# Performance work log

Measured on AMD Instinct MI355X. Metric: run time of the kernel, lower is better.

Reference implementation:

```python
import jax, jax.numpy as jnp
import numpy as np

V, NSEG, MAXLEN, D, H = 32000, 2, 512, 768, 12
HS = D // H  # head_size = 64
B, T, NMASK = 16, 512, 20
LN_EPS = 1e-5


def setup_inputs() -> dict:
    key = jax.random.key(0)
    ks = jax.random.split(key, 16)
    s = 0.02
    return {
        "sequence": jax.random.randint(ks[0], (B, T), 0, V),
        "segment": jax.random.randint(ks[1], (B, T), 0, NSEG),
        "attn_mask": jax.random.randint(ks[2], (B, T), 0, 2).astype(jnp.int32),
        "masked_pos": jax.random.randint(ks[3], (B, NMASK), 0, T),
        "tok_emb": jax.random.normal(ks[4], (V, D), jnp.float32) * s,
        "seg_emb": jax.random.normal(ks[5], (NSEG, D), jnp.float32) * s,
        "pos_emb": jax.random.normal(ks[6], (MAXLEN, D), jnp.float32) * s,
        "ln_g": jnp.ones((D,), jnp.float32),
        "ln_b": jnp.zeros((D,), jnp.float32),
        "Wq": jax.random.normal(ks[7], (H, D, HS), jnp.float32) * s,
        "Wk": jax.random.normal(ks[8], (H, D, HS), jnp.float32) * s,
        "Wv": jax.random.normal(ks[9], (H, D, HS), jnp.float32) * s,
        "W_lm": jax.random.normal(ks[10], (D, V), jnp.float32) * s,
        "b_lm": jnp.zeros((V,), jnp.float32),
        "W_cls": jax.random.normal(ks[11], (D, 2), jnp.float32) * s,
        "b_cls": jnp.zeros((2,), jnp.float32),
    }


def reference(sequence, segment, attn_mask, masked_pos,
              tok_emb, seg_emb, pos_emb, ln_g, ln_b,
              Wq, Wk, Wv, W_lm, b_lm, W_cls, b_cls):
    Tlen = sequence.shape[1]
    # --- BERTEmbedding (dropout = identity in eval) ---
    emb = tok_emb[sequence] + seg_emb[segment] + pos_emb[jnp.arange(Tlen)][None]  # [B,T,D]
    mu = jnp.mean(emb, axis=-1, keepdims=True)
    var = jnp.mean(jnp.square(emb - mu), axis=-1, keepdims=True)
    x = (emb - mu) * jax.lax.rsqrt(var + LN_EPS) * ln_g + ln_b  # [B,T,D]

    # --- Multi-head attention (heads batched instead of Python loop) ---
    q = jnp.einsum('btd,hds->bhts', x, Wq)
    k = jnp.einsum('btd,hds->bhts', x, Wk)
    v = jnp.einsum('btd,hds->bhts', x, Wv)
    wei = jnp.einsum('bhts,bhus->bhtu', q, k) * (HS ** -0.5)  # [B,H,T,T]
    # original: wei.masked_fill(attn_mask[:, :, None] == 0, -1e-11) -> masks over query dim
    wei = jnp.where(attn_mask[:, None, :, None] == 0, jnp.float32(-1e-11), wei)
    wei = jax.nn.softmax(wei, axis=-1)
    out = jnp.einsum('bhtu,bhus->bhts', wei, v)  # [B,H,T,HS]
    x = out.transpose(0, 2, 1, 3).reshape(out.shape[0], Tlen, H * HS)  # cat heads -> [B,T,D]

    # --- Output heads ---
    x_masked = jnp.take_along_axis(x, masked_pos[:, :, None], axis=1)  # [B,NMASK,D]
    logits_lm = x_masked @ W_lm + b_lm          # [B,NMASK,V]
    logits_clsf = x[:, 0, :] @ W_cls + b_cls    # [B,2]
    return (logits_lm, logits_clsf)
```

## Files before the change

kernel.cpp:

```cpp
#include <hip/hip_runtime.h>
#include <hip/hip_bf16.h>

#define V_     32000
#define NSEG_  2
#define MAXLEN_ 512
#define D_     768
#define H_     12
#define HS_    64
#define B_     16
#define T_     512
#define NMASK_ 20
#define LN_EPS_ 1e-5f

typedef __hip_bfloat16 bf16;
typedef unsigned short ushortT;
typedef __attribute__((ext_vector_type(8))) short short8;
typedef __attribute__((ext_vector_type(4))) float f32x4;
typedef __attribute__((ext_vector_type(4))) unsigned int u32x4;
typedef __attribute__((ext_vector_type(4))) unsigned short u16x4;

__device__ __forceinline__ ushortT f2bu(float f) {
    bf16 h = __float2bfloat16(f);
    return *reinterpret_cast<ushortT*>(&h);
}

__global__ void k_embed_ln(const int* __restrict__ seq, const int* __restrict__ seg,
                           const float* __restrict__ tok, const float* __restrict__ sege,
                           const float* __restrict__ pos, const float* __restrict__ g,
                           const float* __restrict__ bb, ushortT* __restrict__ xb) {
    int row = blockIdx.x;
    int t = row & (T_ - 1);
    int tid = threadIdx.x;
    __shared__ float wsum[3], wsq[3];

    int sidx = seq[row];
    int gidx = seg[row];

    f32x4 e = *(const f32x4*)(tok  + (size_t)sidx * D_ + tid * 4);
    f32x4 e2 = *(const f32x4*)(sege + (size_t)gidx * D_ + tid * 4);
    f32x4 e3 = *(const f32x4*)(pos  + (size_t)t    * D_ + tid * 4);
    e = e + e2 + e3;

    float ls = e.x + e.y + e.z + e.w;
    float lq = e.x * e.x + e.y * e.y + e.z * e.z + e.w * e.w;
    #pragma unroll
    for (int o = 32; o > 0; o >>= 1) {
        ls += __shfl_down(ls, o);
        lq += __shfl_down(lq, o);
    }
    if ((tid & 63) == 0) { wsum[tid >> 6] = ls; wsq[tid >> 6] = lq; }
    __syncthreads();
    float s  = wsum[0] + wsum[1] + wsum[2];
    float sq = wsq[0] + wsq[1] + wsq[2];
    float mean = s * (1.0f / D_);
    float var  = sq * (1.0f / D_) - mean * mean;
    float rstd = rsqrtf(var + LN_EPS_);

    f32x4 g4 = *(const f32x4*)(g  + tid * 4);
    f32x4 b4 = *(const f32x4*)(bb + tid * 4);
    f32x4 x4;
    x4.x = (e.x - mean) * rstd * g4.x + b4.x;
    x4.y = (e.y - mean) * rstd * g4.y + b4.y;
    x4.z = (e.z - mean) * rstd * g4.z + b4.z;
    x4.w = (e.w - mean) * rstd * g4.w + b4.w;
    u16x4 ov = {f2bu(x4.x), f2bu(x4.y), f2bu(x4.z), f2bu(x4.w)};
    *(u16x4*)(xb + (size_t)row * D_ + tid * 4) = ov;
}

__global__ void k_prep_wqkv(const float* __restrict__ Wq, const float* __restrict__ Wk,
                            const float* __restrict__ Wv, ushortT* __restrict__ Wt) {
    int blk = blockIdx.x;
    int which = blk / H_, h = blk % H_;
    int kc = blockIdx.y * 64;
    const float* W = (which == 0) ? Wq : (which == 1) ? Wk : Wv;
    __shared__ float tile[64][65];
    int tid = threadIdx.x, c = tid & 63, rgrp = tid >> 6;
    for (int kk = rgrp; kk < 64; kk += 4)
        tile[kk][c] = W[((size_t)h * D_ + kc + kk) * HS_ + c];
    __syncthreads();
    for (int ss = rgrp; ss < 64; ss += 4)
        Wt[((size_t)which * D_ + h * HS_ + ss) * D_ + kc + c] = f2bu(tile[c][ss]);
}

__global__ void k_transpose_lm(const float* __restrict__ W, ushortT* __restrict__ Wt) {
    __shared__ float tile[64][65];
    int v0 = blockIdx.x * 64, d0 = blockIdx.y * 64;
    int tid = threadIdx.x, c = tid & 63;
    for (int rr = tid >> 6; rr < 64; rr += 4)
        tile[rr][c] = W[(size_t)(d0 + rr) * V_ + v0 + c];
    __syncthreads();
    for (int rr = tid >> 6; rr < 64; rr += 4)
        Wt[(size_t)(v0 + rr) * D_ + d0 + c] = f2bu(tile[c][rr]);
}

__global__ void k_gather_xm(const float* __restrict__ x2, const int* __restrict__ masked_pos,
                            ushortT* __restrict__ xm) {
    int r = blockIdx.x;
    int tid = threadIdx.x;
    if (r < B_ * NMASK_) {
        int b = r / NMASK_, m = r % NMASK_;
        int t = masked_pos[b * NMASK_ + m];
        for (int d = tid; d < D_; d += 256)
            xm[(size_t)r * D_ + d] = f2bu(x2[((size_t)b * T_ + t) * D_ + d]);
    } else {
        for (int d = tid; d < D_; d += 256)
            xm[(size_t)r * D_ + d] = 0;
    }
}

__device__ __forceinline__ void stage_tile(const ushortT* __restrict__ A,
                                           const ushortT* __restrict__ Bt,
                                           int m0, int n0, int k0,
                                           ushortT* As, ushortT* Bs,
                                           int w, int lane) {
    #pragma unroll
    for (int i = 0; i < 2; ++i) {
        int slot = w * 64 + lane + i * 256;
        int row = slot >> 2;
        int cs = ((slot & 3) ^ (row & 3)) * 8;
        __builtin_amdgcn_global_load_lds(
            (const __attribute__((address_space(1))) void*)(A + (size_t)(m0 + row) * D_ + k0 + cs),
            (__attribute__((address_space(3))) void*)(As + (w * 64 + i * 256) * 8),
            16, 0, 0);
        __builtin_amdgcn_global_load_lds(
            (const __attribute__((address_space(1))) void*)(Bt + (size_t)(n0 + row) * D_ + k0 + cs),
            (__attribute__((address_space(3))) void*)(Bs + (w * 64 + i * 256) * 8),
            16, 0, 0);
    }
}

__device__ __forceinline__ void gemm128_2ph(const ushortT* __restrict__ A,
                                            const ushortT* __restrict__ Bt,
                                            int m0, int n0,
                                            ushortT* lds,
                                            f32x4 acc[4][4]) {
    const int NT = D_ / 32;
    int tid = threadIdx.x;
    int lane = tid & 63, w = tid >> 6;
    int wr = (w >> 1) * 64, wc = (w & 1) * 64;
    int l16 = lane & 15, lk = lane >> 4;
    int sw = (lk ^ (l16 & 3)) * 8;

    #pragma unroll
    for (int i = 0; i < 4; ++i)
        #pragma unroll
        for (int j = 0; j < 4; ++j)
            acc[i][j] = (f32x4){0.f, 0.f, 0.f, 0.f};

    stage_tile(A, Bt, m0, n0, 0, lds, lds + 4096, w, lane);
    asm volatile("s_waitcnt vmcnt(0)" ::: "memory");
    __builtin_amdgcn_s_barrier();

    for (int t = 0; t < NT; ++t) {
        int cur = (t & 1) * 8192;
        int nxt = 8192 - cur;
        if (t + 1 < NT)
            stage_tile(A, Bt, m0, n0, (t + 1) * 32, lds + nxt, lds + nxt + 4096, w, lane);

        const ushortT* Asc = lds + cur;
        const ushortT* Bsc = lds + cur + 4096;
        short8 a[4], bfr[4];
        #pragma unroll
        for (int i = 0; i < 4; ++i) {
            a[i]   = *(const short8*)(Asc + (wr + i * 16 + l16) * 32 + sw);
            bfr[i] = *(const short8*)(Bsc + (wc + i * 16 + l16) * 32 + sw);
        }
        #pragma unroll
        for (int i = 0; i < 4; ++i)
            #pragma unroll
            for (int j = 0; j < 4; ++j)
                acc[i][j] = __builtin_amdgcn_mfma_f32_16x16x32_bf16(a[i], bfr[j], acc[i][j], 0, 0, 0);

        asm volatile("s_waitcnt vmcnt(0)" ::: "memory");
        __builtin_amdgcn_s_barrier();
    }
}

__global__ __launch_bounds__(256, 4)
void k_gemm_qkv(const ushortT* __restrict__ xb, const ushortT* __restrict__ WcatT,
                ushortT* __restrict__ qb, ushortT* __restrict__ kb,
                ushortT* __restrict__ vb) {
    __shared__ ushortT lds[128 * 136];
    f32x4 acc[4][4];
    int lin = (blockIdx.x & 7) * 144 + (blockIdx.x >> 3);
    int n0 = (lin % 18) * 128, m0 = (lin / 18) * 128;
    gemm128_2ph(xb, WcatT, m0, n0, lds, acc);

    int tid = threadIdx.x;
    int lane = tid & 63, w = tid >> 6;
    int wr = (w >> 1) * 64, wc = (w & 1) * 64;
    int l16 = lane & 15, lk = lane >> 4;

    #pragma unroll
    for (int j = 0; j < 4; ++j) {
        int n = wc + j * 16 + l16;
        #pragma unroll
        for (int i = 0; i < 4; ++i) {
            #pragma unroll
            for (int r = 0; r < 4; ++r) {
                int m = wr + i * 16 + lk * 4 + r;
                lds[m * 136 + n] = f2bu(acc[i][j][r]);
            }
        }
    }
    __syncthreads();

    int which = n0 / D_;
    int nrem0 = n0 - which * D_;
    ushortT* outp = (which == 0) ? qb : (which == 1) ? kb : vb;
    int b = m0 >> 9;
    int t0 = m0 & (T_ - 1);
    #pragma unroll
    for (int p = 0; p < 8; ++p) {
        int chunk = p * 256 + tid;
        int row = chunk >> 4;
        int nc = (chunk & 15) * 8;
        int h = (nrem0 >> 6) + (nc >> 6);
        int s0 = nc & 63;
        u32x4 v = *(const u32x4*)(&lds[row * 136 + nc]);
        *(u32x4*)(outp + ((size_t)(b * H_ + h) * T_ + (t0 + row)) * HS_ + s0) = v;
    }
}

__global__ __launch_bounds__(256, 4)
void k_gemm_lm(const ushortT* __restrict__ xm, const ushortT* __restrict__ WlmT,
               const float* __restrict__ blm, float* __restrict__ out) {
    __shared__ ushortT lds[16384];
    f32x4 acc[4][4];
    int m0 = blockIdx.x * 128, n0 = blockIdx.y * 128;
    gemm128_2ph(xm, WlmT, m0, n0, lds, acc);

    int lane = threadIdx.x & 63, w = threadIdx.x >> 6;
    int wr = (w >> 1) * 64, wc = (w & 1) * 64;
    int l16 = lane & 15, lk = lane >> 4;
    #pragma unroll
    for (int j = 0; j < 4; ++j) {
        int n = n0 + wc + j * 16 + l16;
        float bias = blm[n];
        #pragma unroll
        for (int i = 0; i < 4; ++i) {
            #pragma unroll
            for (int r = 0; r < 4; ++r) {
                int m = m0 + wr + i * 16 + lk * 4 + r;
                if (m < B_ * NMASK_)
                    out[(size_t)m * V_ + n] = acc[i][j][r] + bias;
            }
        }
    }
}

__global__ __launch_bounds__(256, 4)
void k_attn_mfma(const ushortT* __restrict__ qb, const ushortT* __restrict__ kb,
                 const ushortT* __restrict__ vb, const int* __restrict__ attn_mask,
                 float* __restrict__ x2) {
    int lin = (blockIdx.x & 7) * 192 + (blockIdx.x >> 3);
    int qt = lin & 7, bh = lin >> 3;
    int b = bh / H_, h = bh % H_;
    int tid = threadIdx.x, lane = tid & 63, w = tid >> 6;
    int l16 = lane & 15, lk = lane >> 4;

    __shared__ ushortT QP[64][72];
    __shared__ ushortT Ks[64][72];
    __shared__ ushortT Vts[64][72];
    __shared__ float mskS[64];

    const ushortT* Qg = qb + ((size_t)bh * T_ + qt * 64) * HS_;
    #pragma unroll
    for (int i = 0; i < 2; ++i) {
        int slot = tid + i * 256;
        int r = slot >> 3, c8 = (slot & 7) * 8;
        *(u32x4*)(&QP[r][c8]) = *(const u32x4*)(Qg + (size_t)r * HS_ + c8);
    }
    if (tid < 64)
        mskS[tid] = attn_mask[b * T_ + qt * 64 + tid] ? 0.125f : 0.0f;
    __syncthreads();

    short8 aq[2];
    #pragma unroll
    for (int ks = 0; ks < 2; ++ks)
        aq[ks] = *(const short8*)(&QP[w * 16 + l16][ks * 32 + lk * 8]);
    float mrow[4];
    #pragma unroll
    for (int r = 0; r < 4; ++r)
        mrow[r] = mskS[w * 16 + lk * 4 + r];

    float lsum[4];
    f32x4 accO[4];
    #pragma unroll
    for (int r = 0; r < 4; ++r) lsum[r] = 0.f;
    #pragma unroll
    for (int j = 0; j < 4; ++j)
        accO[j] = (f32x4){0.f, 0.f, 0.f, 0.f};

    for (int kt = 0; kt < 8; ++kt) {
        __syncthreads();
        {
            int r = tid >> 2, c = (tid & 3) * 16;
            const ushortT* Kg = kb + ((size_t)bh * T_ + kt * 64 + r) * HS_ + c;
            *(u32x4*)(&Ks[r][c])     = *(const u32x4*)(Kg);
            *(u32x4*)(&Ks[r][c + 8]) = *(const u32x4*)(Kg + 8);
        }
        {
            int r = lane;
            int c = w * 16;
            const ushortT* Vg = vb + ((size_t)bh * T_ + kt * 64 + r) * HS_ + c;
            short8 v0 = *(const short8*)(Vg);
            short8 v1 = *(const short8*)(Vg + 8);
            #pragma unroll
            for (int e = 0; e < 8; ++e) Vts[c + e][r]     = (ushortT)v0[e];
            #pragma unroll
            for (int e = 0; e < 8; ++e) Vts[c + 8 + e][r] = (ushortT)v1[e];
        }
        __syncthreads();

        f32x4 accS[4];
        #pragma unroll
        for (int j = 0; j < 4; ++j)
            accS[j] = (f32x4){0.f, 0.f, 0.f, 0.f};
        #pragma unroll
        for (int ks = 0; ks < 2; ++ks) {
            short8 bk[4];
            #pragma unroll
            for (int j = 0; j < 4; ++j)
                bk[j] = *(const short8*)(&Ks[j * 16 + l16][ks * 32 + lk * 8]);
            #pragma unroll
            for (int j = 0; j < 4; ++j)
                accS[j] = __builtin_amdgcn_mfma_f32_16x16x32_bf16(aq[ks], bk[j], accS[j], 0, 0, 0);
        }

        #pragma unroll
        for (int r = 0; r < 4; ++r) {
            int rowl = lk * 4 + r;
            float m = mrow[r];
            float p0 = __expf(accS[0][r] * m);
            float p1 = __expf(accS[1][r] * m);
            float p2 = __expf(accS[2][r] * m);
            float p3 = __expf(accS[3][r] * m);
            lsum[r] += (p0 + p1) + (p2 + p3);
            QP[w * 16 + rowl][0 * 16 + l16] = f2bu(p0);
            QP[w * 16 + rowl][1 * 16 + l16] = f2bu(p1);
            QP[w * 16 + rowl][2 * 16 + l16] = f2bu(p2);
            QP[w * 16 + rowl][3 * 16 + l16] = f2bu(p3);
        }

        #pragma unroll
        for (int ks2 = 0; ks2 < 2; ++ks2) {
            short8 ap = *(const short8*)(&QP[w * 16 + l16][ks2 * 32 + lk * 8]);
            short8 bv[4];
            #pragma unroll
            for (int j = 0; j < 4; ++j)
                bv[j] = *(const short8*)(&Vts[j * 16 + l16][ks2 * 32 + lk * 8]);
            #pragma unroll
            for (int j = 0; j < 4; ++j)
                accO[j] = __builtin_amdgcn_mfma_f32_16x16x32_bf16(ap, bv[j], accO[j], 0, 0, 0);
        }
    }

    #pragma unroll
    for (int r = 0; r < 4; ++r) {
        float s = lsum[r];
        #pragma unroll
        for (int off = 1; off < 16; off <<= 1)
            s += __shfl_xor(s, off);
        float inv = 1.0f / s;
        int t = qt * 64 + w * 16 + lk * 4 + r;
        float* outp = x2 + ((size_t)b * T_ + t) * D_ + h * HS_;
        #pragma unroll
        for (int j = 0; j < 4; ++j)
            outp[j * 16 + l16] = accO[j][r] * inv;
    }
}

__global__ void k_cls(const float* __restrict__ x2, const float* __restrict__ Wc,
                      const float* __restrict__ bc, float* __restrict__ out) {
    int b = blockIdx.x;
    int tid = threadIdx.x;
    __shared__ float red0[4], red1[4];
    float a0 = 0.f, a1 = 0.f;
    const float* xr = x2 + (size_t)b * T_ * D_;
    for (int d = tid; d < D_; d += 256) {
        float x = xr[d];
        a0 += x * Wc[d * 2];
        a1 += x * Wc[d * 2 + 1];
    }
    #pragma unroll
    for (int o = 32; o > 0; o >>= 1) {
        a0 += __shfl_down(a0, o);
        a1 += __shfl_down(a1, o);
    }
    if ((tid & 63) == 0) { red0[tid >> 6] = a0; red1[tid >> 6] = a1; }
    __syncthreads();
    if (tid == 0)
        out[b * 2]     = red0[0] + red0[1] + red0[2] + red0[3] + bc[0];
    if (tid == 1)
        out[b * 2 + 1] = red1[0] + red1[1] + red1[2] + red1[3] + bc[1];
}

extern "C" void kernel_launch(void* const* d_in, const int* in_sizes, int n_in,
                              void* d_out, int out_size, void* d_ws, size_t ws_size,
                              hipStream_t stream) {
    const int* seq        = (const int*)d_in[0];
    const int* seg        = (const int*)d_in[1];
    const int* attn_mask  = (const int*)d_in[2];
    const int* masked_pos = (const int*)d_in[3];
    const float* tok  = (const float*)d_in[4];
    const float* sege = (const float*)d_in[5];
    const float* pos  = (const float*)d_in[6];
    const float* ln_g = (const float*)d_in[7];
    const float* ln_b = (const float*)d_in[8];
    const float* Wq   = (const float*)d_in[9];
    const float* Wk   = (const float*)d_in[10];
    const float* Wv   = (const float*)d_in[11];
    const float* Wlm  = (const float*)d_in[12];
    const float* blm  = (const float*)d_in[13];
    const float* Wc   = (const float*)d_in[14];
    const float* bc   = (const float*)d_in[15];

    float* out_lm  = (float*)d_out;
    float* out_cls = out_lm + (size_t)B_ * NMASK_ * V_;

    const size_t XSZ = (size_t)B_ * T_ * D_;
    float* ws = (float*)d_ws;
    float*   x2   = ws;
    ushortT* base = (ushortT*)(ws + XSZ);
    ushortT* xb    = base;
    ushortT* qb    = base + XSZ;
    ushortT* kb    = base + 2 * XSZ;
    ushortT* vb    = base + 3 * XSZ;
    ushortT* WcatT = base + 4 * XSZ;
    ushortT* WlmT  = base;
    ushortT* xm    = base + (size_t)V_ * D_;

    k_embed_ln<<<B_ * T_, 192, 0, stream>>>(seq, seg, tok, sege, pos, ln_g, ln_b, xb);
    k_prep_wqkv<<<dim3(3 * H_, 12), 256, 0, stream>>>(Wq, Wk, Wv, WcatT);
    k_gemm_qkv<<<1152, 256, 0, stream>>>(xb, WcatT, qb, kb, vb);
    k_attn_mfma<<<192 * 8, 256, 0, stream>>>(qb, kb, vb, attn_mask, x2);
    k_transpose_lm<<<dim3(V_ / 64, D_ / 64), 256, 0, stream>>>(Wlm, WlmT);
    k_gather_xm<<<384, 256, 0, stream>>>(x2, masked_pos, xm);
    k_gemm_lm<<<dim3(3, 250), 256, 0, stream>>>(xm, WlmT, blm, out_lm);
    k_cls<<<B_, 256, 0, stream>>>(x2, Wc, bc, out_cls);
}
```

Baseline: 163.4 us.

## Fuse LM weight transpose and bf16 conversion into LM GEMM loader

Removes the separate kernel that transposed and converted the 768x32000 fp32 LM weight to bf16. The LM GEMM now reads the fp32 weights directly, converts them to bf16 in registers and writes them transposed into padded LDS, overlapping these loads with the MFMA work. This avoids a full write and re-read of a bf16 copy of the weight. The trade-off is that each of the 3 M-blocks reads the fp32 weight itself (three times the fp32 traffic through L2), and the loads are scalar and strided by V rather than vector loads into LDS.

```diff
diff --git a/kernel.cpp b/kernel.cpp
--- a/kernel.cpp
+++ b/kernel.cpp
@@ -82,17 +82,6 @@
         Wt[((size_t)which * D_ + h * HS_ + ss) * D_ + kc + c] = f2bu(tile[c][ss]);
 }
 
-__global__ void k_transpose_lm(const float* __restrict__ W, ushortT* __restrict__ Wt) {
-    __shared__ float tile[64][65];
-    int v0 = blockIdx.x * 64, d0 = blockIdx.y * 64;
-    int tid = threadIdx.x, c = tid & 63;
-    for (int rr = tid >> 6; rr < 64; rr += 4)
-        tile[rr][c] = W[(size_t)(d0 + rr) * V_ + v0 + c];
-    __syncthreads();
-    for (int rr = tid >> 6; rr < 64; rr += 4)
-        Wt[(size_t)(v0 + rr) * D_ + d0 + c] = f2bu(tile[c][rr]);
-}
-
 __global__ void k_gather_xm(const float* __restrict__ x2, const int* __restrict__ masked_pos,
                             ushortT* __restrict__ xm) {
     int r = blockIdx.x;
@@ -108,23 +97,16 @@
     }
 }
 
-__device__ __forceinline__ void stage_tile(const ushortT* __restrict__ A,
-                                           const ushortT* __restrict__ Bt,
-                                           int m0, int n0, int k0,
-                                           ushortT* As, ushortT* Bs,
-                                           int w, int lane) {
+__device__ __forceinline__ void stage_chunk(const ushortT* __restrict__ src, int row_stride,
+                                            int r0, int k0, ushortT* dst, int w, int lane) {
     #pragma unroll
     for (int i = 0; i < 2; ++i) {
         int slot = w * 64 + lane + i * 256;
         int row = slot >> 2;
         int cs = ((slot & 3) ^ (row & 3)) * 8;
         __builtin_amdgcn_global_load_lds(
-            (const __attribute__((address_space(1))) void*)(A + (size_t)(m0 + row) * D_ + k0 + cs),
-            (__attribute__((address_space(3))) void*)(As + (w * 64 + i * 256) * 8),
-            16, 0, 0);
-        __builtin_amdgcn_global_load_lds(
-            (const __attribute__((address_space(1))) void*)(Bt + (size_t)(n0 + row) * D_ + k0 + cs),
-            (__attribute__((address_space(3))) void*)(Bs + (w * 64 + i * 256) * 8),
+            (const __attribute__((address_space(1))) void*)(src + (size_t)(r0 + row) * row_stride + k0 + cs),
+            (__attribute__((address_space(3))) void*)(dst + (w * 64 + i * 256) * 8),
             16, 0, 0);
     }
 }
@@ -147,15 +129,18 @@
         for (int j = 0; j < 4; ++j)
             acc[i][j] = (f32x4){0.f, 0.f, 0.f, 0.f};
 
-    stage_tile(A, Bt, m0, n0, 0, lds, lds + 4096, w, lane);
+    stage_chunk(A, D_, m0, 0, lds, w, lane);
+    stage_chunk(Bt, D_, n0, 0, lds + 4096, w, lane);
     asm volatile("s_waitcnt vmcnt(0)" ::: "memory");
     __builtin_amdgcn_s_barrier();
 
     for (int t = 0; t < NT; ++t) {
         int cur = (t & 1) * 8192;
         int nxt = 8192 - cur;
-        if (t + 1 < NT)
-            stage_tile(A, Bt, m0, n0, (t + 1) * 32, lds + nxt, lds + nxt + 4096, w, lane);
+        if (t + 1 < NT) {
+            stage_chunk(A, D_, m0, (t + 1) * 32, lds + nxt, w, lane);
+            stage_chunk(Bt, D_, n0, (t + 1) * 32, lds + nxt + 4096, w, lane);
+        }
 
         const ushortT* Asc = lds + cur;
         const ushortT* Bsc = lds + cur + 4096;
@@ -223,16 +208,82 @@
 }
 
 __global__ __launch_bounds__(256, 4)
-void k_gemm_lm(const ushortT* __restrict__ xm, const ushortT* __restrict__ WlmT,
+void k_gemm_lm(const ushortT* __restrict__ xm, const float* __restrict__ Wlm,
                const float* __restrict__ blm, float* __restrict__ out) {
-    __shared__ ushortT lds[16384];
+    const int NT = D_ / 32;
+    __shared__ ushortT As[2][4096];
+    __shared__ ushortT Bs[2][128 * 36];
     f32x4 acc[4][4];
     int m0 = blockIdx.x * 128, n0 = blockIdx.y * 128;
-    gemm128_2ph(xm, WlmT, m0, n0, lds, acc);
-
-    int lane = threadIdx.x & 63, w = threadIdx.x >> 6;
+
+    int tid = threadIdx.x;
+    int lane = tid & 63, w = tid >> 6;
     int wr = (w >> 1) * 64, wc = (w & 1) * 64;
     int l16 = lane & 15, lk = lane >> 4;
+    int sw = (lk ^ (l16 & 3)) * 8;
+    int n_l = tid & 127;
+    int kkg = tid >> 7;
+
+    #pragma unroll
+    for (int i = 0; i < 4; ++i)
+        #pragma unroll
+        for (int j = 0; j < 4; ++j)
+            acc[i][j] = (f32x4){0.f, 0.f, 0.f, 0.f};
+
+    stage_chunk(xm, D_, m0, 0, As[0], w, lane);
+    {
+        #pragma unroll
+        for (int g = 0; g < 4; ++g) {
+            int kk0 = (g * 2 + kkg) * 4;
+            const float* Wp = Wlm + (size_t)kk0 * V_ + n0 + n_l;
+            u16x4 pk = {f2bu(Wp[0]), f2bu(Wp[(size_t)V_]), f2bu(Wp[(size_t)2 * V_]), f2bu(Wp[(size_t)3 * V_])};
+            *(u16x4*)(&Bs[0][n_l * 36 + kk0]) = pk;
+        }
+    }
+    asm volatile("s_waitcnt vmcnt(0) lgkmcnt(0)" ::: "memory");
+    __builtin_amdgcn_s_barrier();
+
+    for (int t = 0; t < NT; ++t) {
+        int cur = t & 1, nx = cur ^ 1;
+        float bf[16];
+        if (t + 1 < NT) {
+            stage_chunk(xm, D_, m0, (t + 1) * 32, As[nx], w, lane);
+            int k0 = (t + 1) * 32;
+            #pragma unroll
+            for (int g = 0; g < 4; ++g) {
+                int kk0 = (g * 2 + kkg) * 4;
+                const float* Wp = Wlm + (size_t)(k0 + kk0) * V_ + n0 + n_l;
+                bf[g * 4 + 0] = Wp[0];
+                bf[g * 4 + 1] = Wp[(size_t)V_];
+                bf[g * 4 + 2] = Wp[(size_t)2 * V_];
+                bf[g * 4 + 3] = Wp[(size_t)3 * V_];
+            }
+        }
+
+        short8 a[4], bfr[4];
+        #pragma unroll
+        for (int i = 0; i < 4; ++i) {
+            a[i]   = *(const short8*)(&As[cur][(wr + i * 16 + l16) * 32 + sw]);
+            bfr[i] = *(const short8*)(&Bs[cur][(wc + i * 16 + l16) * 36 + lk * 8]);
+        }
+        #pragma unroll
+        for (int i = 0; i < 4; ++i)
+            #pragma unroll
+            for (int j = 0; j < 4; ++j)
+                acc[i][j] = __builtin_amdgcn_mfma_f32_16x16x32_bf16(a[i], bfr[j], acc[i][j], 0, 0, 0);
+
+        if (t + 1 < NT) {
+            #pragma unroll
+            for (int g = 0; g < 4; ++g) {
+                int kk0 = (g * 2 + kkg) * 4;
+                u16x4 pk = {f2bu(bf[g * 4]), f2bu(bf[g * 4 + 1]), f2bu(bf[g * 4 + 2]), f2bu(bf[g * 4 + 3])};
+                *(u16x4*)(&Bs[nx][n_l * 36 + kk0]) = pk;
+            }
+        }
+        asm volatile("s_waitcnt vmcnt(0) lgkmcnt(0)" ::: "memory");
+        __builtin_amdgcn_s_barrier();
+    }
+
     #pragma unroll
     for (int j = 0; j < 4; ++j) {
         int n = n0 + wc + j * 16 + l16;
@@ -428,15 +479,13 @@
     ushortT* kb    = base + 2 * XSZ;
     ushortT* vb    = base + 3 * XSZ;
     ushortT* WcatT = base + 4 * XSZ;
-    ushortT* WlmT  = base;
-    ushortT* xm    = base + (size_t)V_ * D_;
+    ushortT* xm    = base;
 
     k_embed_ln<<<B_ * T_, 192, 0, stream>>>(seq, seg, tok, sege, pos, ln_g, ln_b, xb);
     k_prep_wqkv<<<dim3(3 * H_, 12), 256, 0, stream>>>(Wq, Wk, Wv, WcatT);
     k_gemm_qkv<<<1152, 256, 0, stream>>>(xb, WcatT, qb, kb, vb);
     k_attn_mfma<<<192 * 8, 256, 0, stream>>>(qb, kb, vb, attn_mask, x2);
-    k_transpose_lm<<<dim3(V_ / 64, D_ / 64), 256, 0, stream>>>(Wlm, WlmT);
     k_gather_xm<<<384, 256, 0, stream>>>(x2, masked_pos, xm);
-    k_gemm_lm<<<dim3(3, 250), 256, 0, stream>>>(xm, WlmT, blm, out_lm);
+    k_gemm_lm<<<dim3(3, 250), 256, 0, stream>>>(xm, Wlm, blm, out_lm);
     k_cls<<<B_, 256, 0, stream>>>(x2, Wc, bc, out_cls);
 }
```

New measurement: 158.0 us. 1.03x faster.
